# Performance work log

Measured on AMD Instinct MI355X. Metric: run time of the kernel, lower is better.

The kernel has to match this reference:

```python
import jax, jax.numpy as jnp
import numpy as np

N = 16384   # total gate nodes (64 graphs x 256 gates)
B = 64      # graphs in batch
E = 49152   # directed edges (avg in-degree 3)
Q = 32      # qubit_num
F = 256     # feat_dim
D = 2 * F   # node feature dim = 512
H = 2       # heads
A = 128     # action_num


def _gatv2(x, wl, wr, att, b, src, dst, n):
    # PyG GATv2Conv (concat=True, share_weights=False, negative_slope=0.2)
    h, c = att.shape
    xl = (x @ wl).reshape(n, h, c)   # source-side projection [N,H,C]
    xr = (x @ wr).reshape(n, h, c)   # target-side projection [N,H,C]
    e = jax.nn.leaky_relu(xl[src] + xr[dst], 0.2)       # [E,H,C]
    logit = jnp.einsum('ehc,hc->eh', e, att)             # [E,H]
    m = jax.ops.segment_max(logit, dst, num_segments=n)  # softmax over in-edges per target
    p = jnp.exp(logit - m[dst])
    den = jax.ops.segment_sum(p, dst, num_segments=n)
    alpha = p / den[dst]                                 # [E,H]
    out = jax.ops.segment_sum(alpha[:, :, None] * xl[src], dst, num_segments=n)
    return out.reshape(n, h * c) + b


def _forward(x, xt_w1, xt_b1, xt_w2, xt_b2,
             g0_wl, g0_wr, g0_att, g0_b,
             g1_wl, g1_wr, g1_att, g1_b,
             g2_wl, g2_wr, g2_att, g2_b,
             g3_wl, g3_wr, g3_att, g3_b,
             g4_wl, g4_wr, g4_att, g4_b,
             ln_w, ln_b, aggr_t,
             m_w1, m_b1, m_w2, m_b2, m_w3, m_b3,
             edge_index, batch):
    lr = lambda v: jax.nn.leaky_relu(v, 0.01)
    # x_trans: Linear -> LeakyReLU -> Linear, then fold qubit-pairs into one node
    h0 = lr(x @ xt_w1 + xt_b1) @ xt_w2 + xt_b2           # [2N, F]
    cx = h0.reshape(-1, D)                               # [N, 2F]
    n = cx.shape[0]
    # GATv2Conv default add_self_loops=True (inputs contain no self loops)
    sl = jnp.arange(n, dtype=edge_index.dtype)
    src = jnp.concatenate([edge_index[0], sl])
    dst = jnp.concatenate([edge_index[1], sl])
    res = cx
    h = lr(_gatv2(cx, g0_wl, g0_wr, g0_att, g0_b, src, dst, n))
    for wl_, wr_, att_, b_ in ((g1_wl, g1_wr, g1_att, g1_b),
                               (g2_wl, g2_wr, g2_att, g2_b),
                               (g3_wl, g3_wr, g3_att, g3_b)):
        h = lr(_gatv2(h, wl_, wr_, att_, b_, src, dst, n))
    h = lr(_gatv2(h, g4_wl, g4_wr, g4_att, g4_b, src, dst, n))
    h = h + res                                           # residual [N, 2F]
    # PyG LayerNorm(mode='graph'): normalize over nodes AND channels per graph
    cnt = jax.ops.segment_sum(jnp.ones((n,), h.dtype), batch, num_segments=B)
    norm = cnt * h.shape[1]
    mean = jax.ops.segment_sum(h.sum(-1), batch, num_segments=B) / norm
    hc = h - mean[batch][:, None]
    var = jax.ops.segment_sum((hc * hc).sum(-1), batch, num_segments=B) / norm
    h = hc / jnp.sqrt(var + 1e-5)[batch][:, None] * ln_w + ln_b
    # SoftmaxAggregation(learn=True): channel-wise softmax over nodes per graph
    logit = h * aggr_t
    mg = jax.ops.segment_max(logit, batch, num_segments=B)
    p = jnp.exp(logit - mg[batch])
    den = jax.ops.segment_sum(p, batch, num_segments=B)
    g = jax.ops.segment_sum((p / den[batch]) * h, batch, num_segments=B)  # [B, 2F]
    # head MLP 512->384->256->128
    o = lr(g @ m_w1 + m_b1)
    o = lr(o @ m_w2 + m_b2)
    return o @ m_w3 + m_b3


def setup_inputs() -> dict:
    key = jax.random.key(0)
    ks = iter(jax.random.split(key, 64))
    def rn(shp, s=0.05):
        return jax.random.normal(next(ks), shp, jnp.float32) * s
    d = {}
    d['x'] = jax.random.normal(next(ks), (2 * N, Q), jnp.float32)
    src = jax.random.randint(next(ks), (E,), 0, N, jnp.int32)
    off = jax.random.randint(next(ks), (E,), 1, N, jnp.int32)
    d['edge_index'] = jnp.stack([src, (src + off) % N])  # no self loops
    d['batch'] = jnp.arange(N, dtype=jnp.int32) // (N // B)
    d['xt_w1'] = rn((Q, F)); d['xt_b1'] = rn((F,))
    d['xt_w2'] = rn((F, F)); d['xt_b2'] = rn((F,))
    d['g0_wl'] = rn((D, H * D)); d['g0_wr'] = rn((D, H * D))
    d['g0_att'] = rn((H, D));    d['g0_b'] = rn((H * D,))
    for i in (1, 2, 3):
        d[f'g{i}_wl'] = rn((H * D, H * D)); d[f'g{i}_wr'] = rn((H * D, H * D))
        d[f'g{i}_att'] = rn((H, D));        d[f'g{i}_b'] = rn((H * D,))
    d['g4_wl'] = rn((H * D, D)); d['g4_wr'] = rn((H * D, D))
    d['g4_att'] = rn((1, D));    d['g4_b'] = rn((D,))
    d['ln_w'] = jnp.ones((D,), jnp.float32); d['ln_b'] = jnp.zeros((D,), jnp.float32)
    d['aggr_t'] = jnp.array(1.0, jnp.float32)
    d['m_w1'] = rn((D, 384)); d['m_b1'] = rn((384,))
    d['m_w2'] = rn((384, 256)); d['m_b2'] = rn((256,))
    d['m_w3'] = rn((256, A)); d['m_b3'] = rn((A,))
    return d


def reference(x, edge_index, batch, xt_w1, xt_b1, xt_w2, xt_b2,
              g0_wl, g0_wr, g0_att, g0_b,
              g1_wl, g1_wr, g1_att, g1_b,
              g2_wl, g2_wr, g2_att, g2_b,
              g3_wl, g3_wr, g3_att, g3_b,
              g4_wl, g4_wr, g4_att, g4_b,
              ln_w, ln_b, aggr_t,
              m_w1, m_b1, m_w2, m_b2, m_w3, m_b3):
    return _forward(x, xt_w1, xt_b1, xt_w2, xt_b2,
                    g0_wl, g0_wr, g0_att, g0_b,
                    g1_wl, g1_wr, g1_att, g1_b,
                    g2_wl, g2_wr, g2_att, g2_b,
                    g3_wl, g3_wr, g3_att, g3_b,
                    g4_wl, g4_wr, g4_att, g4_b,
                    ln_w, ln_b, aggr_t,
                    m_w1, m_b1, m_w2, m_b2, m_w3, m_b3,
                    edge_index, batch)
```

## Files before the change

kernel.cpp:

```cpp
#include <hip/hip_runtime.h>
#include <hip/hip_bf16.h>

typedef __hip_bfloat16 bf16;

#define NN 16384
#define BBG 64
#define EE 49152
#define ET (EE + NN)
#define DD 512
#define NG (NN / BBG)

__device__ __forceinline__ float b2f(bf16 v) { return __bfloat162float(v); }
__device__ __forceinline__ bf16 f2b(float v) { return __float2bfloat16(v); }
__device__ __forceinline__ float sb2f(short s) {
    unsigned u = ((unsigned)(unsigned short)s) << 16;
    return __builtin_bit_cast(float, u);
}
__device__ __forceinline__ short f2bs(float v) {
    bf16 b = f2b(v);
    return __builtin_bit_cast(short, b);
}
__device__ __forceinline__ int clampi(int v, int lo, int hi)
{
    return v < lo ? lo : (v > hi ? hi : v);
}

__device__ __forceinline__ unsigned char enc_e4m3(float y)
{
    unsigned b = __builtin_bit_cast(unsigned, y);
    unsigned s = (b >> 31) << 7;
    float a = fabsf(y);
    unsigned ab = b & 0x7fffffffu;
    unsigned rb = ab + (1u << 19);
    int e = (int)(rb >> 23) - 120;
    unsigned m = (rb >> 20) & 7u;
    unsigned qn = (unsigned)(e << 3) | m;
    if (qn > 126u) qn = 126u;
    unsigned qd = (unsigned)__float2int_rn(a * 512.f);
    unsigned q = (a < 0.015625f) ? qd : qn;
    return (unsigned char)(q | s);
}
__device__ __forceinline__ float dec_e4m3(unsigned q)
{
    unsigned e = (q >> 3) & 15u, m = q & 7u;
    float nrm = __builtin_bit_cast(float, ((e + 120u) << 23) | (m << 20));
    float dnm = (float)m * 0.001953125f;
    float v = e ? nrm : dnm;
    return (q & 128u) ? -v : v;
}

typedef __attribute__((ext_vector_type(8))) short bf16x8;
typedef __attribute__((ext_vector_type(4))) float f32x4;

#define AS1 __attribute__((address_space(1)))
#define AS3 __attribute__((address_space(3)))

__global__ __launch_bounds__(256) void gemm_mfma_bt(
    const bf16* __restrict__ A, const bf16* __restrict__ Bt,
    const float* __restrict__ bias, bf16* __restrict__ Cb,
    int M, int N, int K, float slope, int has_act)
{
    __shared__ bf16 As[128 * 32];
    __shared__ bf16 Bs[128 * 32];
    const int tid = threadIdx.x;
    const int w = tid >> 6;
    const int l = tid & 63;
    const int bm = blockIdx.y * 128;
    const int bn = blockIdx.x * 128;
    const int wrow = (w >> 1) * 64;
    const int wcol = (w & 1) * 64;
    const int quad = l >> 4;
    const int c16 = l & 15;

    const int lrow = l >> 2;
    const int lchunk = l & 3;
    const bf16* Ag = A + (size_t)(bm + w * 16 + lrow) * K + lchunk * 8;
    const bf16* Bg = Bt + (size_t)(bn + w * 16 + lrow) * K + lchunk * 8;
    char* AsB = (char*)As;
    char* BsB = (char*)Bs;

    f32x4 acc[4][4] = {};

    for (int k0 = 0; k0 < K; k0 += 32) {
        __builtin_amdgcn_global_load_lds((const AS1 void*)(Ag + k0),
            (AS3 void*)(AsB + w * 1024), 16, 0, 0);
        __builtin_amdgcn_global_load_lds((const AS1 void*)(Ag + (size_t)64 * K + k0),
            (AS3 void*)(AsB + 4096 + w * 1024), 16, 0, 0);
        __builtin_amdgcn_global_load_lds((const AS1 void*)(Bg + k0),
            (AS3 void*)(BsB + w * 1024), 16, 0, 0);
        __builtin_amdgcn_global_load_lds((const AS1 void*)(Bg + (size_t)64 * K + k0),
            (AS3 void*)(BsB + 4096 + w * 1024), 16, 0, 0);
        __syncthreads();

        bf16x8 a[4], b[4];
#pragma unroll
        for (int i = 0; i < 4; i++) {
            int ra = wrow + i * 16 + c16;
            a[i] = *(const bf16x8*)(AsB + ra * 64 + quad * 16);
            int rb = wcol + i * 16 + c16;
            b[i] = *(const bf16x8*)(BsB + rb * 64 + quad * 16);
        }
#pragma unroll
        for (int i = 0; i < 4; i++)
#pragma unroll
            for (int j = 0; j < 4; j++)
                acc[i][j] = __builtin_amdgcn_mfma_f32_16x16x32_bf16(
                    a[i], b[j], acc[i][j], 0, 0, 0);
        __syncthreads();
    }

#pragma unroll
    for (int i = 0; i < 4; i++) {
#pragma unroll
        for (int j = 0; j < 4; j++) {
            int col = bn + wcol + j * 16 + c16;
            float bv = bias ? bias[col] : 0.f;
#pragma unroll
            for (int r = 0; r < 4; r++) {
                int row = bm + wrow + i * 16 + quad * 4 + r;
                float v = acc[i][j][r] + bv;
                if (has_act) v = (v >= 0.f) ? v : v * slope;
                Cb[(size_t)row * N + col] = f2b(v);
            }
        }
    }
}

__global__ __launch_bounds__(256) void gemm_mfma_dual(
    const bf16* __restrict__ A, const bf16* __restrict__ Bt,
    bf16* __restrict__ X0b, unsigned char* __restrict__ X0q,
    bf16* __restrict__ X0s, bf16* __restrict__ X1,
    int M, int K, int HC, int quant)
{
    __shared__ bf16 As[128 * 32];
    __shared__ bf16 Bs[128 * 32];
    const int tid = threadIdx.x;
    const int w = tid >> 6;
    const int l = tid & 63;
    const int bm = blockIdx.y * 128;
    const int bn = blockIdx.x * 128;
    const int wrow = (w >> 1) * 64;
    const int wcol = (w & 1) * 64;
    const int quad = l >> 4;
    const int c16 = l & 15;

    const int lrow = l >> 2;
    const int lchunk = l & 3;
    const bf16* Ag = A + (size_t)(bm + w * 16 + lrow) * K + lchunk * 8;
    const bf16* Bg = Bt + (size_t)(bn + w * 16 + lrow) * K + lchunk * 8;
    char* AsB = (char*)As;
    char* BsB = (char*)Bs;

    f32x4 acc[4][4] = {};

    for (int k0 = 0; k0 < K; k0 += 32) {
        __builtin_amdgcn_global_load_lds((const AS1 void*)(Ag + k0),
            (AS3 void*)(AsB + w * 1024), 16, 0, 0);
        __builtin_amdgcn_global_load_lds((const AS1 void*)(Ag + (size_t)64 * K + k0),
            (AS3 void*)(AsB + 4096 + w * 1024), 16, 0, 0);
        __builtin_amdgcn_global_load_lds((const AS1 void*)(Bg + k0),
            (AS3 void*)(BsB + w * 1024), 16, 0, 0);
        __builtin_amdgcn_global_load_lds((const AS1 void*)(Bg + (size_t)64 * K + k0),
            (AS3 void*)(BsB + 4096 + w * 1024), 16, 0, 0);
        __syncthreads();

        bf16x8 a[4], b[4];
#pragma unroll
        for (int i = 0; i < 4; i++) {
            int ra = wrow + i * 16 + c16;
            a[i] = *(const bf16x8*)(AsB + ra * 64 + quad * 16);
            int rb = wcol + i * 16 + c16;
            b[i] = *(const bf16x8*)(BsB + rb * 64 + quad * 16);
        }
#pragma unroll
        for (int i = 0; i < 4; i++)
#pragma unroll
            for (int j = 0; j < 4; j++)
                acc[i][j] = __builtin_amdgcn_mfma_f32_16x16x32_bf16(
                    a[i], b[j], acc[i][j], 0, 0, 0);
        __syncthreads();
    }

#pragma unroll
    for (int i = 0; i < 4; i++) {
#pragma unroll
        for (int j = 0; j < 4; j++) {
            int col = bn + wcol + j * 16 + c16;
            if (col < HC) {
                if (quant) {
#pragma unroll
                    for (int r = 0; r < 4; r++) {
                        int row = bm + wrow + i * 16 + quad * 4 + r;
                        float v = acc[i][j][r];
                        float mx = fabsf(v);
#pragma unroll
                        for (int msk = 8; msk; msk >>= 1)
                            mx = fmaxf(mx, __shfl_xor(mx, msk));
                        float sc = b2f(f2b(fmaxf(mx, 1e-20f) * (1.f / 448.f)));
                        unsigned char q = enc_e4m3(v * (1.f / sc));
                        X0q[(size_t)row * HC + col] = q;
                        if (c16 == 0)
                            X0s[(size_t)row * (HC / 16) + (col >> 4)] = f2b(sc);
                    }
                } else {
#pragma unroll
                    for (int r = 0; r < 4; r++) {
                        int row = bm + wrow + i * 16 + quad * 4 + r;
                        X0b[(size_t)row * HC + col] = f2b(acc[i][j][r]);
                    }
                }
            } else {
#pragma unroll
                for (int r = 0; r < 4; r++) {
                    int row = bm + wrow + i * 16 + quad * 4 + r;
                    X1[(size_t)row * HC + col - HC] = f2b(acc[i][j][r]);
                }
            }
        }
    }
}

__global__ __launch_bounds__(256) void gemm_f32(
    const float* __restrict__ A, const float* __restrict__ W,
    const float* __restrict__ bias, float* __restrict__ C,
    int M, int N, int K, float slope, int has_act)
{
    const int BK = 16;
    __shared__ float Asm[BK][64 + 1];
    __shared__ float Wsm[BK][64 + 1];
    int tid = threadIdx.x;
    int bm = blockIdx.y * 64;
    int bn = blockIdx.x * 64;
    int tr = tid >> 4;
    int tc = tid & 15;
    float acc[4][4] = {};

    for (int k0 = 0; k0 < K; k0 += BK) {
        {
            int col = tid & 15;
            int row = tid >> 4;
#pragma unroll
            for (int p = 0; p < 4; p++) {
                int r = row + p * 16;
                Asm[col][r] = A[(size_t)(bm + r) * K + k0 + col];
            }
        }
        {
            int wc = tid & 63;
            int wr = tid >> 6;
#pragma unroll
            for (int p = 0; p < 4; p++) {
                int r = wr + p * 4;
                Wsm[r][wc] = W[(size_t)(k0 + r) * N + bn + wc];
            }
        }
        __syncthreads();
#pragma unroll
        for (int kk = 0; kk < BK; kk++) {
            float a[4], w[4];
#pragma unroll
            for (int i = 0; i < 4; i++) a[i] = Asm[kk][tr * 4 + i];
#pragma unroll
            for (int j = 0; j < 4; j++) w[j] = Wsm[kk][tc * 4 + j];
#pragma unroll
            for (int i = 0; i < 4; i++)
#pragma unroll
                for (int j = 0; j < 4; j++)
                    acc[i][j] += a[i] * w[j];
        }
        __syncthreads();
    }
#pragma unroll
    for (int i = 0; i < 4; i++) {
        int r = bm + tr * 4 + i;
#pragma unroll
        for (int j = 0; j < 4; j++) {
            int cn = bn + tc * 4 + j;
            float v = acc[i][j];
            if (bias) v += bias[cn];
            if (has_act) v = (v >= 0.f) ? v : v * slope;
            C[(size_t)r * N + cn] = v;
        }
    }
}

struct TPackAll {
    const float* in[12];
    bf16* out[12];
    int R[12], C[12];
};

__global__ __launch_bounds__(256) void transpose_batch(TPackAll pk)
{
    int z = blockIdx.z;
    int R = pk.R[z], C = pk.C[z];
    int c0 = blockIdx.x * 32;
    int r0 = blockIdx.y * 32;
    if (c0 >= C || r0 >= R) return;
    const float* in = pk.in[z];
    bf16* out = pk.out[z];
    __shared__ float tile[32][33];
    int tx = threadIdx.x & 31;
    int ty = threadIdx.x >> 5;
#pragma unroll
    for (int k = 0; k < 4; k++) {
        int r = ty + k * 8;
        tile[r][tx] = in[(size_t)(r0 + r) * C + c0 + tx];
    }
    __syncthreads();
#pragma unroll
    for (int k = 0; k < 4; k++) {
        int rr = ty + k * 8;
        out[(size_t)(c0 + rr) * R + r0 + tx] = f2b(tile[tx][rr]);
    }
}

__global__ void f2b_vec(const float* __restrict__ in, bf16* __restrict__ out, int n)
{
    int i = blockIdx.x * 256 + threadIdx.x;
    if (i < n) out[i] = f2b(in[i]);
}

__global__ void count_deg(const int* __restrict__ ei, int* __restrict__ deg)
{
    int e = blockIdx.x * 256 + threadIdx.x;
    if (e >= ET) return;
    int d = (e < EE) ? ei[EE + e] : (e - EE);
    d = clampi(d, 0, NN - 1);
    atomicAdd(&deg[d], 1);
}

__global__ __launch_bounds__(256) void scan_deg(const int* __restrict__ deg,
                                                int* __restrict__ rs)
{
    __shared__ int part[256];
    __shared__ int psum[257];
    int tid = threadIdx.x;
    const int per = NN / 256;
    int base = tid * per;
    int s = 0;
    for (int i = 0; i < per; i++) s += deg[base + i];
    part[tid] = s;
    __syncthreads();
    if (tid == 0) {
        int acc = 0;
        for (int i = 0; i < 256; i++) { psum[i] = acc; acc += part[i]; }
        psum[256] = acc;
    }
    __syncthreads();
    int acc = psum[tid];
    for (int i = 0; i < per; i++) { rs[base + i] = acc; acc += deg[base + i]; }
    if (tid == 0) rs[NN] = psum[256];
}

__global__ void fill_csr(const int* __restrict__ ei, const int* __restrict__ rs,
                         int* __restrict__ cur, int* __restrict__ csrc)
{
    int e = blockIdx.x * 256 + threadIdx.x;
    if (e >= ET) return;
    int s, d;
    if (e < EE) { s = ei[e]; d = ei[EE + e]; } else { s = d = e - EE; }
    s = clampi(s, 0, NN - 1);
    d = clampi(d, 0, NN - 1);
    int pos = atomicAdd(&cur[d], 1);
    int slot = clampi(rs[d] + pos, 0, ET - 1);
    csrc[slot] = s;
}

__global__ __launch_bounds__(256, 4) void gat_q(
    const unsigned char* __restrict__ xlq, const bf16* __restrict__ xls,
    const bf16* __restrict__ xr, const float* __restrict__ att,
    const float* __restrict__ bias, const int* __restrict__ rs,
    const int* __restrict__ csrc, bf16* __restrict__ out_b)
{
    constexpr int HC = 1024, CPL = 16;
    const int tid = threadIdx.x;
    const int w = tid >> 6;
    const int lane = tid & 63;
    const int n = blockIdx.x * 4 + w;
    const int c0 = lane * CPL;

    int start = rs[n];
    int deg = clampi(rs[n + 1] - start, 1, 64);
    start = clampi(start, 0, ET - 1);
    int my_src = 0;
    if (lane < deg) my_src = clampi(csrc[start + lane], 0, NN - 1);

    float av[CPL], rv[CPL];
    {
        bf16x8 r0 = *(const bf16x8*)(xr + (size_t)n * HC + c0);
        bf16x8 r1 = *(const bf16x8*)(xr + (size_t)n * HC + c0 + 8);
#pragma unroll
        for (int k = 0; k < 8; k++) { rv[k] = sb2f(r0[k]); rv[8 + k] = sb2f(r1[k]); }
#pragma unroll
        for (int k = 0; k < CPL; k++) av[k] = att[c0 + k];
    }

    float m = -1e30f, den = 0.f;
    float acc[CPL];
#pragma unroll
    for (int k = 0; k < CPL; k++) acc[k] = 0.f;

    auto loadrow = [&](int i, uint4& q, float& sc) {
        int s = __shfl(my_src, i);
        q = *(const uint4*)(xlq + (size_t)s * HC + c0);
        sc = b2f(xls[(size_t)s * 64 + lane]);
    };
    auto process = [&](const uint4& q, float sc) {
        float x[CPL];
        const unsigned* qw = (const unsigned*)&q;
#pragma unroll
        for (int k = 0; k < CPL; k++)
            x[k] = dec_e4m3((qw[k >> 2] >> ((k & 3) * 8)) & 255u) * sc;
        float part = 0.f;
#pragma unroll
        for (int k = 0; k < CPL; k++) {
            float u = x[k] + rv[k];
            u = (u >= 0.f) ? u : 0.2f * u;
            part = fmaf(av[k], u, part);
        }
#pragma unroll
        for (int msk = 16; msk; msk >>= 1) part += __shfl_xor(part, msk);
        float lg = part;
        float mn = fmaxf(m, lg);
        float r = __expf(m - mn);
        float pi = __expf(lg - mn);
        m = mn;
        den = den * r + pi;
#pragma unroll
        for (int k = 0; k < CPL; k++) acc[k] = fmaf(acc[k], r, pi * x[k]);
    };

    uint4 cq, q1, q2, qn;
    float cs, s1, s2, sn;
    loadrow(0, cq, cs);
    if (deg > 1) loadrow(1, q1, s1);
    if (deg > 2) loadrow(2, q2, s2);
    for (int i = 0; i < deg; i++) {
        if (i + 3 < deg) loadrow(i + 3, qn, sn);
        process(cq, cs);
        cq = q1; cs = s1; q1 = q2; s1 = s2; q2 = qn; s2 = sn;
    }

    float inv = 1.f / den;
    bf16x8 ov0, ov1;
#pragma unroll
    for (int k = 0; k < 8; k++) {
        float v = fmaf(acc[k], inv, bias[c0 + k]);
        v = (v >= 0.f) ? v : 0.01f * v;
        ov0[k] = f2bs(v);
        float v2 = fmaf(acc[8 + k], inv, bias[c0 + 8 + k]);
        v2 = (v2 >= 0.f) ? v2 : 0.01f * v2;
        ov1[k] = f2bs(v2);
    }
    *(bf16x8*)(out_b + (size_t)n * HC + c0) = ov0;
    *(bf16x8*)(out_b + (size_t)n * HC + c0 + 8) = ov1;
}

template<int HC>
__global__ __launch_bounds__(256) void gat_b(
    const bf16* __restrict__ xl, const bf16* __restrict__ xr,
    const float* __restrict__ att, const float* __restrict__ bias,
    const int* __restrict__ rs, const int* __restrict__ csrc,
    const bf16* __restrict__ res, bf16* __restrict__ out_b,
    float* __restrict__ lnsums)
{
    constexpr int CPL = HC / 64;
    constexpr int NV = CPL / 8;
    const int tid = threadIdx.x;
    const int w = tid >> 6;
    const int lane = tid & 63;
    const int n = blockIdx.x * 4 + w;
    const int c0 = lane * CPL;

    int start = rs[n];
    int deg = clampi(rs[n + 1] - start, 1, 64);
    start = clampi(start, 0, ET - 1);
    int my_src = 0;
    if (lane < deg) my_src = clampi(csrc[start + lane], 0, NN - 1);

    float av[CPL], rv[CPL];
    {
        bf16x8 rp[NV];
#pragma unroll
        for (int v = 0; v < NV; v++)
            rp[v] = *(const bf16x8*)(xr + (size_t)n * HC + c0 + v * 8);
#pragma unroll
        for (int k = 0; k < CPL; k++) {
            rv[k] = sb2f(rp[k / 8][k % 8]);
            av[k] = att[c0 + k];
        }
    }

    float m = -1e30f, den = 0.f;
    float acc[CPL];
#pragma unroll
    for (int k = 0; k < CPL; k++) acc[k] = 0.f;

    auto loadrow = [&](int i, bf16x8* dst) {
        int s = __shfl(my_src, i);
        const bf16* rp = xl + (size_t)s * HC + c0;
#pragma unroll
        for (int v = 0; v < NV; v++) dst[v] = *(const bf16x8*)(rp + v * 8);
    };

    bf16x8 cur[NV], nx1[NV], nx2[NV];
    loadrow(0, cur);
    if (deg > 1) loadrow(1, nx1);
    if (deg > 2) loadrow(2, nx2);

    for (int i = 0; i < deg; i++) {
        bf16x8 nxt[NV];
        if (i + 3 < deg) loadrow(i + 3, nxt);

        float part = 0.f;
#pragma unroll
        for (int k = 0; k < CPL; k++) {
            float x = sb2f(cur[k / 8][k % 8]);
            float u = x + rv[k];
            u = (u >= 0.f) ? u : 0.2f * u;
            part = fmaf(av[k], u, part);
        }
        if (HC == 1024) {
#pragma unroll
            for (int msk = 16; msk; msk >>= 1) part += __shfl_xor(part, msk);
        } else {
#pragma unroll
            for (int msk = 32; msk; msk >>= 1) part += __shfl_xor(part, msk);
        }
        float lg = part;
        float mn = fmaxf(m, lg);
        float r = __expf(m - mn);
        float pi = __expf(lg - mn);
        m = mn;
        den = den * r + pi;
#pragma unroll
        for (int k = 0; k < CPL; k++) {
            float x = sb2f(cur[k / 8][k % 8]);
            acc[k] = fmaf(acc[k], r, pi * x);
        }
#pragma unroll
        for (int v = 0; v < NV; v++) { cur[v] = nx1[v]; nx1[v] = nx2[v]; nx2[v] = nxt[v]; }
    }

    float inv = 1.f / den;
    float ls = 0.f, ls2 = 0.f;
    float vals[CPL];
#pragma unroll
    for (int k = 0; k < CPL; k++) {
        float v = fmaf(acc[k], inv, bias[c0 + k]);
        v = (v >= 0.f) ? v : 0.01f * v;
        vals[k] = v;
    }
    if (res) {
        bf16x8 rr[NV];
#pragma unroll
        for (int v = 0; v < NV; v++)
            rr[v] = *(const bf16x8*)(res + (size_t)n * HC + c0 + v * 8);
#pragma unroll
        for (int k = 0; k < CPL; k++) {
            vals[k] += sb2f(rr[k / 8][k % 8]);
            ls += vals[k];
            ls2 += vals[k] * vals[k];
        }
    }
#pragma unroll
    for (int v = 0; v < NV; v++) {
        bf16x8 ov;
#pragma unroll
        for (int k = 0; k < 8; k++) ov[k] = f2bs(vals[v * 8 + k]);
        *(bf16x8*)(out_b + (size_t)n * HC + c0 + v * 8) = ov;
    }

    if (lnsums) {
#pragma unroll
        for (int msk = 32; msk; msk >>= 1) {
            ls += __shfl_xor(ls, msk);
            ls2 += __shfl_xor(ls2, msk);
        }
        if (lane == 0) {
            int g = n >> 8;
            atomicAdd(&lnsums[g], ls);
            atomicAdd(&lnsums[BBG + g], ls2);
        }
    }
}

__global__ __launch_bounds__(256) void aggr_partial(
    const bf16* __restrict__ h, const float* __restrict__ lnsums,
    const float* __restrict__ lnw, const float* __restrict__ lnb,
    const float* __restrict__ t_, float* __restrict__ pm,
    float* __restrict__ pd, float* __restrict__ pa)
{
    int g = blockIdx.x, ch = blockIdx.y, nk = blockIdx.z;
    int tid = threadIdx.x;
    int c = ch * 256 + tid;
    const float tot = (float)(NG * DD);
    float S = lnsums[g], S2 = lnsums[BBG + g];
    float mu = S / tot;
    float iv = rsqrtf(fmaxf(S2 / tot - mu * mu, 0.f) + 1e-5f);
    float w = lnw[c], b = lnb[c], t = t_[0];
    size_t base = (size_t)g * NG * DD + (size_t)nk * 32 * DD + c;
    float m = -1e30f, den = 0.f, acc = 0.f;
    for (int i = 0; i < 32; i++) {
        float hn = (b2f(h[base + (size_t)i * DD]) - mu) * iv * w + b;
        float lg = hn * t;
        if (lg > m) {
            float r = __expf(m - lg);
            den *= r; acc *= r; m = lg;
        }
        float p = __expf(lg - m);
        den += p; acc += p * hn;
    }
    size_t idx = (((size_t)g * 2 + ch) * 8 + nk) * 256 + tid;
    pm[idx] = m; pd[idx] = den; pa[idx] = acc;
}

__global__ __launch_bounds__(256) void aggr_combine(
    const float* __restrict__ pm, const float* __restrict__ pd,
    const float* __restrict__ pa, float* __restrict__ gout)
{
    int g = blockIdx.x, ch = blockIdx.y;
    int tid = threadIdx.x;
    size_t base = (((size_t)g * 2 + ch) * 8) * 256 + tid;
    float m = -1e30f;
#pragma unroll
    for (int k = 0; k < 8; k++) m = fmaxf(m, pm[base + k * 256]);
    float den = 0.f, acc = 0.f;
#pragma unroll
    for (int k = 0; k < 8; k++) {
        float r = __expf(pm[base + k * 256] - m);
        den += pd[base + k * 256] * r;
        acc += pa[base + k * 256] * r;
    }
    gout[(size_t)g * DD + ch * 256 + tid] = acc / den;
}

extern "C" void kernel_launch(void* const* d_in, const int* in_sizes, int n_in,
                              void* d_out, int out_size, void* d_ws, size_t ws_size,
                              hipStream_t stream)
{
    const float* x      = (const float*)d_in[0];
    const int*   ei     = (const int*)d_in[1];
    const float* xt_w1  = (const float*)d_in[3];
    const float* xt_b1  = (const float*)d_in[4];
    const float* xt_w2  = (const float*)d_in[5];
    const float* xt_b2  = (const float*)d_in[6];
    const float* ln_w   = (const float*)d_in[27];
    const float* ln_b   = (const float*)d_in[28];
    const float* aggr_t = (const float*)d_in[29];
    const float* m_w1   = (const float*)d_in[30];
    const float* m_b1   = (const float*)d_in[31];
    const float* m_w2   = (const float*)d_in[32];
    const float* m_b2   = (const float*)d_in[33];
    const float* m_w3   = (const float*)d_in[34];
    const float* m_b3   = (const float*)d_in[35];
    float* out = (float*)d_out;

    char* p = (char*)d_ws;
    auto take = [&](size_t bytes) {
        char* r = p;
        p += (bytes + 255) & ~(size_t)255;
        return r;
    };
    int* i_deg     = (int*)take((size_t)(NN + 1) * 4);
    int* i_rs      = (int*)take((size_t)(NN + 1) * 4);
    int* i_cur     = (int*)take((size_t)NN * 4);
    int* i_src     = (int*)take((size_t)ET * 4);
    float* f_sums  = (float*)take((size_t)2 * BBG * 4);
    float* f_pm    = (float*)take((size_t)BBG * 2 * 8 * 256 * 4);
    float* f_pd    = (float*)take((size_t)BBG * 2 * 8 * 256 * 4);
    float* f_pa    = (float*)take((size_t)BBG * 2 * 8 * 256 * 4);
    float* b_g     = (float*)take((size_t)BBG * DD * 4);
    float* b_m1    = (float*)take((size_t)BBG * 384 * 4);
    float* b_m2    = (float*)take((size_t)BBG * 256 * 4);
    bf16* b_resb   = (bf16*)take((size_t)NN * DD * 2);
    bf16* b_h      = (bf16*)take((size_t)NN * DD * 2);
    bf16* b_hb     = (bf16*)take((size_t)NN * 1024 * 2);
    bf16* b_xlb    = (bf16*)take((size_t)NN * 1024 * 2);
    bf16* b_xrb    = (bf16*)take((size_t)NN * 1024 * 2);
    unsigned char* b_xlq = (unsigned char*)take((size_t)NN * 1024);
    bf16* b_xls    = (bf16*)take((size_t)NN * 64 * 2);
    bf16* b_xb     = (bf16*)take((size_t)2 * NN * 32 * 2);
    bf16* b_wcat   = (bf16*)take((size_t)8 * 1024 * 1024 * 2);
    bf16* b_w1b    = (bf16*)take((size_t)32 * 256 * 2);
    bf16* b_w2b    = (bf16*)take((size_t)256 * 256 * 2);
    bf16* b_t1b = b_hb;

    size_t woff[5], wlen[5];
    {
        size_t o = 0;
        for (int L = 0; L < 5; L++) {
            int Fin = (L == 0) ? 512 : 1024;
            int HC  = (L == 4) ? 512 : 1024;
            woff[L] = o;
            wlen[L] = (size_t)2 * HC * Fin;
            o += wlen[L];
        }
    }

    dim3 blk(256);

    hipMemsetAsync(i_deg, 0, (size_t)(NN + 1) * 4, stream);
    hipMemsetAsync(i_cur, 0, (size_t)NN * 4, stream);
    hipMemsetAsync(f_sums, 0, (size_t)2 * BBG * 4, stream);
    count_deg<<<ET / 256, blk, 0, stream>>>(ei, i_deg);
    scan_deg<<<1, blk, 0, stream>>>(i_deg, i_rs);
    fill_csr<<<ET / 256, blk, 0, stream>>>(ei, i_rs, i_cur, i_src);

    f2b_vec<<<(2 * NN * 32 + 255) / 256, blk, 0, stream>>>(x, b_xb, 2 * NN * 32);
    {
        TPackAll pk;
        pk.in[0] = xt_w1; pk.out[0] = b_w1b; pk.R[0] = 32;  pk.C[0] = 256;
        pk.in[1] = xt_w2; pk.out[1] = b_w2b; pk.R[1] = 256; pk.C[1] = 256;
        for (int L = 0; L < 5; L++) {
            int Fin = (L == 0) ? 512 : 1024;
            int HC  = (L == 4) ? 512 : 1024;
            pk.in[2 + 2 * L] = (const float*)d_in[7 + 4 * L];
            pk.out[2 + 2 * L] = b_wcat + woff[L];
            pk.R[2 + 2 * L] = Fin; pk.C[2 + 2 * L] = HC;
            pk.in[3 + 2 * L] = (const float*)d_in[8 + 4 * L];
            pk.out[3 + 2 * L] = b_wcat + woff[L] + (size_t)HC * Fin;
            pk.R[3 + 2 * L] = Fin; pk.C[3 + 2 * L] = HC;
        }
        transpose_batch<<<dim3(32, 32, 12), blk, 0, stream>>>(pk);
    }

    gemm_mfma_bt<<<dim3(256 / 128, 32768 / 128), blk, 0, stream>>>(
        b_xb, b_w1b, xt_b1, b_t1b, 32768, 256, 32, 0.01f, 1);
    gemm_mfma_bt<<<dim3(256 / 128, 32768 / 128), blk, 0, stream>>>(
        b_t1b, b_w2b, xt_b2, b_resb, 32768, 256, 256, 0.f, 0);

    for (int L = 0; L < 5; L++) {
        const float* att = (const float*)d_in[9 + 4 * L];
        const float* gb  = (const float*)d_in[10 + 4 * L];
        int Fin = (L == 0) ? 512 : 1024;
        int HC  = (L == 4) ? 512 : 1024;
        int quant = (L <= 2) ? 1 : 0;
        const bf16* hin = (L == 0) ? b_resb : b_hb;

        gemm_mfma_dual<<<dim3(2 * HC / 128, NN / 128), blk, 0, stream>>>(
            hin, b_wcat + woff[L],
            quant ? (bf16*)nullptr : b_xlb, b_xlq, b_xls, b_xrb,
            NN, Fin, HC, quant);
        if (L <= 2) {
            gat_q<<<NN / 4, blk, 0, stream>>>(
                b_xlq, b_xls, b_xrb, att, gb, i_rs, i_src, b_hb);
        } else if (L == 3) {
            gat_b<1024><<<NN / 4, blk, 0, stream>>>(
                b_xlb, b_xrb, att, gb, i_rs, i_src,
                (const bf16*)nullptr, b_hb, (float*)nullptr);
        } else {
            gat_b<512><<<NN / 4, blk, 0, stream>>>(
                b_xlb, b_xrb, att, gb, i_rs, i_src,
                b_resb, b_h, f_sums);
        }
    }

    aggr_partial<<<dim3(BBG, 2, 8), blk, 0, stream>>>(
        b_h, f_sums, ln_w, ln_b, aggr_t, f_pm, f_pd, f_pa);
    aggr_combine<<<dim3(BBG, 2), blk, 0, stream>>>(f_pm, f_pd, f_pa, b_g);

    gemm_f32<<<dim3(384 / 64, 1), blk, 0, stream>>>(
        b_g, m_w1, m_b1, b_m1, 64, 384, 512, 0.01f, 1);
    gemm_f32<<<dim3(256 / 64, 1), blk, 0, stream>>>(
        b_m1, m_w2, m_b2, b_m2, 64, 256, 384, 0.01f, 1);
    gemm_f32<<<dim3(128 / 64, 1), blk, 0, stream>>>(
        b_m2, m_w3, m_b3, out, 64, 128, 256, 0.f, 0);
}
```

Measured before the change: 1.163 ms.

## Move FP8 quantization of xl out of GEMM epilogue into separate kernel; quantize layer 3 too

The dual GEMM now always writes bf16 xl, and a new quant_rows kernel reads each row and produces e4m3 bytes plus per-16 bf16 scales with vectorized stores. This replaces the byte-scattered, shuffle-heavy quantizing epilogue in the GEMM. Layer 3 now also takes the FP8 gather path (gat_q) instead of the bf16 gat_b<1024>, which halves its gather traffic. The cost is an extra kernel launch per layer and a full bf16 write and read of xl, plus more quantization error on layer 3.

```diff
diff --git a/kernel.cpp b/kernel.cpp
--- a/kernel.cpp
+++ b/kernel.cpp
@@ -128,9 +128,8 @@
 
 __global__ __launch_bounds__(256) void gemm_mfma_dual(
     const bf16* __restrict__ A, const bf16* __restrict__ Bt,
-    bf16* __restrict__ X0b, unsigned char* __restrict__ X0q,
-    bf16* __restrict__ X0s, bf16* __restrict__ X1,
-    int M, int K, int HC, int quant)
+    bf16* __restrict__ X0, bf16* __restrict__ X1,
+    int M, int K, int HC)
 {
     __shared__ bf16 As[128 * 32];
     __shared__ bf16 Bs[128 * 32];
@@ -186,38 +185,45 @@
 #pragma unroll
         for (int j = 0; j < 4; j++) {
             int col = bn + wcol + j * 16 + c16;
-            if (col < HC) {
-                if (quant) {
-#pragma unroll
-                    for (int r = 0; r < 4; r++) {
-                        int row = bm + wrow + i * 16 + quad * 4 + r;
-                        float v = acc[i][j][r];
-                        float mx = fabsf(v);
-#pragma unroll
-                        for (int msk = 8; msk; msk >>= 1)
-                            mx = fmaxf(mx, __shfl_xor(mx, msk));
-                        float sc = b2f(f2b(fmaxf(mx, 1e-20f) * (1.f / 448.f)));
-                        unsigned char q = enc_e4m3(v * (1.f / sc));
-                        X0q[(size_t)row * HC + col] = q;
-                        if (c16 == 0)
-                            X0s[(size_t)row * (HC / 16) + (col >> 4)] = f2b(sc);
-                    }
-                } else {
-#pragma unroll
-                    for (int r = 0; r < 4; r++) {
-                        int row = bm + wrow + i * 16 + quad * 4 + r;
-                        X0b[(size_t)row * HC + col] = f2b(acc[i][j][r]);
-                    }
-                }
-            } else {
-#pragma unroll
-                for (int r = 0; r < 4; r++) {
-                    int row = bm + wrow + i * 16 + quad * 4 + r;
-                    X1[(size_t)row * HC + col - HC] = f2b(acc[i][j][r]);
-                }
+            bf16* dst = (col < HC) ? (X0 + col) : (X1 + col - HC);
+#pragma unroll
+            for (int r = 0; r < 4; r++) {
+                int row = bm + wrow + i * 16 + quad * 4 + r;
+                dst[(size_t)row * HC] = f2b(acc[i][j][r]);
             }
         }
     }
+}
+
+__global__ __launch_bounds__(256, 4) void quant_rows(
+    const bf16* __restrict__ xl, unsigned char* __restrict__ xq,
+    bf16* __restrict__ xs)
+{
+    const int n = blockIdx.x * 4 + (threadIdx.x >> 6);
+    const int lane = threadIdx.x & 63;
+    const bf16* rp = xl + (size_t)n * 1024 + lane * 16;
+    bf16x8 v0 = *(const bf16x8*)(rp);
+    bf16x8 v1 = *(const bf16x8*)(rp + 8);
+    float x[16];
+#pragma unroll
+    for (int k = 0; k < 8; k++) { x[k] = sb2f(v0[k]); x[8 + k] = sb2f(v1[k]); }
+    float mx = 0.f;
+#pragma unroll
+    for (int k = 0; k < 16; k++) mx = fmaxf(mx, fabsf(x[k]));
+    float sc = b2f(f2b(fmaxf(mx, 1e-20f) * (1.f / 448.f)));
+    float isc = 1.f / sc;
+    uint4 q;
+    unsigned* qw = (unsigned*)&q;
+#pragma unroll
+    for (int w = 0; w < 4; w++) {
+        unsigned pk = 0;
+#pragma unroll
+        for (int b = 0; b < 4; b++)
+            pk |= ((unsigned)enc_e4m3(x[w * 4 + b] * isc)) << (b * 8);
+        qw[w] = pk;
+    }
+    *(uint4*)(xq + (size_t)n * 1024 + lane * 16) = q;
+    xs[(size_t)n * 64 + lane] = f2b(sc);
 }
 
 __global__ __launch_bounds__(256) void gemm_f32(
@@ -457,16 +463,14 @@
     *(bf16x8*)(out_b + (size_t)n * HC + c0 + 8) = ov1;
 }
 
-template<int HC>
-__global__ __launch_bounds__(256) void gat_b(
+__global__ __launch_bounds__(256) void gat_b512(
     const bf16* __restrict__ xl, const bf16* __restrict__ xr,
     const float* __restrict__ att, const float* __restrict__ bias,
     const int* __restrict__ rs, const int* __restrict__ csrc,
     const bf16* __restrict__ res, bf16* __restrict__ out_b,
     float* __restrict__ lnsums)
 {
-    constexpr int CPL = HC / 64;
-    constexpr int NV = CPL / 8;
+    constexpr int HC = 512, CPL = 8;
     const int tid = threadIdx.x;
     const int w = tid >> 6;
     const int lane = tid & 63;
@@ -481,13 +485,10 @@
 
     float av[CPL], rv[CPL];
     {
-        bf16x8 rp[NV];
-#pragma unroll
-        for (int v = 0; v < NV; v++)
-            rp[v] = *(const bf16x8*)(xr + (size_t)n * HC + c0 + v * 8);
+        bf16x8 rp = *(const bf16x8*)(xr + (size_t)n * HC + c0);
 #pragma unroll
         for (int k = 0; k < CPL; k++) {
-            rv[k] = sb2f(rp[k / 8][k % 8]);
+            rv[k] = sb2f(rp[k]);
             av[k] = att[c0 + k];
         }
     }
@@ -497,37 +498,28 @@
 #pragma unroll
     for (int k = 0; k < CPL; k++) acc[k] = 0.f;
 
-    auto loadrow = [&](int i, bf16x8* dst) {
+    auto loadrow = [&](int i, bf16x8& dst) {
         int s = __shfl(my_src, i);
-        const bf16* rp = xl + (size_t)s * HC + c0;
-#pragma unroll
-        for (int v = 0; v < NV; v++) dst[v] = *(const bf16x8*)(rp + v * 8);
+        dst = *(const bf16x8*)(xl + (size_t)s * HC + c0);
     };
 
-    bf16x8 cur[NV], nx1[NV], nx2[NV];
+    bf16x8 cur, nx1, nx2, nxt;
     loadrow(0, cur);
     if (deg > 1) loadrow(1, nx1);
     if (deg > 2) loadrow(2, nx2);
 
     for (int i = 0; i < deg; i++) {
-        bf16x8 nxt[NV];
         if (i + 3 < deg) loadrow(i + 3, nxt);
-
         float part = 0.f;
 #pragma unroll
         for (int k = 0; k < CPL; k++) {
-            float x = sb2f(cur[k / 8][k % 8]);
+            float x = sb2f(cur[k]);
             float u = x + rv[k];
             u = (u >= 0.f) ? u : 0.2f * u;
             part = fmaf(av[k], u, part);
         }
-        if (HC == 1024) {
-#pragma unroll
-            for (int msk = 16; msk; msk >>= 1) part += __shfl_xor(part, msk);
-        } else {
-#pragma unroll
-            for (int msk = 32; msk; msk >>= 1) part += __shfl_xor(part, msk);
-        }
+#pragma unroll
+        for (int msk = 32; msk; msk >>= 1) part += __shfl_xor(part, msk);
         float lg = part;
         float mn = fmaxf(m, lg);
         float r = __expf(m - mn);
@@ -536,11 +528,10 @@
         den = den * r + pi;
 #pragma unroll
         for (int k = 0; k < CPL; k++) {
-            float x = sb2f(cur[k / 8][k % 8]);
+            float x = sb2f(cur[k]);
             acc[k] = fmaf(acc[k], r, pi * x);
         }
-#pragma unroll
-        for (int v = 0; v < NV; v++) { cur[v] = nx1[v]; nx1[v] = nx2[v]; nx2[v] = nxt[v]; }
+        cur = nx1; nx1 = nx2; nx2 = nxt;
     }
 
     float inv = 1.f / den;
@@ -552,37 +543,29 @@
         v = (v >= 0.f) ? v : 0.01f * v;
         vals[k] = v;
     }
-    if (res) {
-        bf16x8 rr[NV];
-#pragma unroll
-        for (int v = 0; v < NV; v++)
-            rr[v] = *(const bf16x8*)(res + (size_t)n * HC + c0 + v * 8);
+    {
+        bf16x8 rr = *(const bf16x8*)(res + (size_t)n * HC + c0);
 #pragma unroll
         for (int k = 0; k < CPL; k++) {
-            vals[k] += sb2f(rr[k / 8][k % 8]);
+            vals[k] += sb2f(rr[k]);
             ls += vals[k];
             ls2 += vals[k] * vals[k];
         }
     }
-#pragma unroll
-    for (int v = 0; v < NV; v++) {
-        bf16x8 ov;
-#pragma unroll
-        for (int k = 0; k < 8; k++) ov[k] = f2bs(vals[v * 8 + k]);
-        *(bf16x8*)(out_b + (size_t)n * HC + c0 + v * 8) = ov;
-    }
-
-    if (lnsums) {
-#pragma unroll
-        for (int msk = 32; msk; msk >>= 1) {
-            ls += __shfl_xor(ls, msk);
-            ls2 += __shfl_xor(ls2, msk);
-        }
-        if (lane == 0) {
-            int g = n >> 8;
-            atomicAdd(&lnsums[g], ls);
-            atomicAdd(&lnsums[BBG + g], ls2);
-        }
+    bf16x8 ov;
+#pragma unroll
+    for (int k = 0; k < 8; k++) ov[k] = f2bs(vals[k]);
+    *(bf16x8*)(out_b + (size_t)n * HC + c0) = ov;
+
+#pragma unroll
+    for (int msk = 32; msk; msk >>= 1) {
+        ls += __shfl_xor(ls, msk);
+        ls2 += __shfl_xor(ls2, msk);
+    }
+    if (lane == 0) {
+        int g = n >> 8;
+        atomicAdd(&lnsums[g], ls);
+        atomicAdd(&lnsums[BBG + g], ls2);
     }
 }
 
@@ -687,15 +670,14 @@
     bf16* b_w2b    = (bf16*)take((size_t)256 * 256 * 2);
     bf16* b_t1b = b_hb;
 
-    size_t woff[5], wlen[5];
+    size_t woff[5];
     {
         size_t o = 0;
         for (int L = 0; L < 5; L++) {
             int Fin = (L == 0) ? 512 : 1024;
             int HC  = (L == 4) ? 512 : 1024;
             woff[L] = o;
-            wlen[L] = (size_t)2 * HC * Fin;
-            o += wlen[L];
+            o += (size_t)2 * HC * Fin;
         }
     }
 
@@ -736,24 +718,17 @@
         const float* gb  = (const float*)d_in[10 + 4 * L];
         int Fin = (L == 0) ? 512 : 1024;
         int HC  = (L == 4) ? 512 : 1024;
-        int quant = (L <= 2) ? 1 : 0;
         const bf16* hin = (L == 0) ? b_resb : b_hb;
 
         gemm_mfma_dual<<<dim3(2 * HC / 128, NN / 128), blk, 0, stream>>>(
-            hin, b_wcat + woff[L],
-            quant ? (bf16*)nullptr : b_xlb, b_xlq, b_xls, b_xrb,
-            NN, Fin, HC, quant);
-        if (L <= 2) {
+            hin, b_wcat + woff[L], b_xlb, b_xrb, NN, Fin, HC);
+        if (L < 4) {
+            quant_rows<<<NN / 4, blk, 0, stream>>>(b_xlb, b_xlq, b_xls);
             gat_q<<<NN / 4, blk, 0, stream>>>(
                 b_xlq, b_xls, b_xrb, att, gb, i_rs, i_src, b_hb);
-        } else if (L == 3) {
-            gat_b<1024><<<NN / 4, blk, 0, stream>>>(
-                b_xlb, b_xrb, att, gb, i_rs, i_src,
-                (const bf16*)nullptr, b_hb, (float*)nullptr);
         } else {
-            gat_b<512><<<NN / 4, blk, 0, stream>>>(
-                b_xlb, b_xrb, att, gb, i_rs, i_src,
-                b_resb, b_h, f_sums);
+            gat_b512<<<NN / 4, blk, 0, stream>>>(
+                b_xlb, b_xrb, att, gb, i_rs, i_src, b_resb, b_h, f_sums);
         }
     }
 
```

Result: faster. 1.086 ms (-6.6%).
